# Kernel optimization log

Measured on AMD Instinct MI355X. Metric: run time of the kernel, lower is better.

Reference implementation:

```python
import jax, jax.numpy as jnp
import numpy as np

N, E = 30000, 480000
IN_DIM, HID, HEADS, OUT_DIM, EDIM = 128, 64, 4, 32, 1
NEG_SLOPE = 0.2
EPS_BN = 1e-5


def segment_softmax(logits, seg, num_segments):
    m = jax.ops.segment_max(logits, seg, num_segments=num_segments)
    ex = jnp.exp(logits - m[seg])
    s = jax.ops.segment_sum(ex, seg, num_segments=num_segments)
    return ex / (s[seg] + 1e-16)


def gat_layer(x, src, dst, ea, W, We, a_s, a_d, a_e, b):
    # PyG GATConv: shared lin for src/dst, edge_dim attention, softmax over dst
    n = x.shape[0]
    H, D = a_s.shape
    h = (x @ W).reshape(n, H, D)                      # [N,H,D]
    e = (ea @ We).reshape(-1, H, D)                   # [E,H,D]
    logits = (h * a_s).sum(-1)[src] + (h * a_d).sum(-1)[dst] + (e * a_e).sum(-1)
    alpha = segment_softmax(jax.nn.leaky_relu(logits, NEG_SLOPE), dst, n)  # [E,H]
    out = jax.ops.segment_sum(alpha[:, :, None] * h[src], dst, num_segments=n)
    return out.reshape(n, H * D) + b


def setup_inputs() -> dict:
    key = jax.random.key(0)
    ks = jax.random.split(key, 24)
    s = 0.1
    return {
        "x": jax.random.normal(ks[0], (N, IN_DIM), jnp.float32),
        "edge_attr": jax.random.uniform(ks[1], (E, EDIM), jnp.float32),
        "bn_gamma": jnp.ones((EDIM,), jnp.float32),
        "bn_beta": jnp.zeros((EDIM,), jnp.float32),
        "W1": s * jax.random.normal(ks[2], (IN_DIM, HEADS * HID), jnp.float32),
        "We1": s * jax.random.normal(ks[3], (EDIM, HEADS * HID), jnp.float32),
        "a_src1": s * jax.random.normal(ks[4], (HEADS, HID), jnp.float32),
        "a_dst1": s * jax.random.normal(ks[5], (HEADS, HID), jnp.float32),
        "a_edge1": s * jax.random.normal(ks[6], (HEADS, HID), jnp.float32),
        "b1": jnp.zeros((HEADS * HID,), jnp.float32),
        "W2": s * jax.random.normal(ks[7], (HEADS * HID, OUT_DIM), jnp.float32),
        "We2": s * jax.random.normal(ks[8], (EDIM, OUT_DIM), jnp.float32),
        "a_src2": s * jax.random.normal(ks[9], (1, OUT_DIM), jnp.float32),
        "a_dst2": s * jax.random.normal(ks[10], (1, OUT_DIM), jnp.float32),
        "a_edge2": s * jax.random.normal(ks[11], (1, OUT_DIM), jnp.float32),
        "b2": jnp.zeros((OUT_DIM,), jnp.float32),
        "dec_W1": s * jax.random.normal(ks[12], (OUT_DIM, HID), jnp.float32),
        "dec_b1": jnp.zeros((HID,), jnp.float32),
        "dec_W2": s * jax.random.normal(ks[13], (HID, IN_DIM), jnp.float32),
        "dec_b2": jnp.zeros((IN_DIM,), jnp.float32),
        "edge_index": jax.random.randint(ks[14], (2, E), 0, N, dtype=jnp.int32),
    }


def reference(x, edge_attr, bn_gamma, bn_beta, W1, We1, a_src1, a_dst1, a_edge1, b1,
              W2, We2, a_src2, a_dst2, a_edge2, b2, dec_W1, dec_b1, dec_W2, dec_b2,
              edge_index):
    n = x.shape[0]
    src, dst = edge_index[0], edge_index[1]
    # BatchNorm1d (batch stats, biased var) on log1p(edge_attr)
    ea = jnp.log1p(edge_attr)
    mu = ea.mean(0)
    var = ea.var(0)
    ea = (ea - mu) / jnp.sqrt(var + EPS_BN) * bn_gamma + bn_beta
    # add_self_loops with fill_value='mean' (mean of incoming edge attrs per node)
    ones = jnp.ones((src.shape[0],), ea.dtype)
    cnt = jax.ops.segment_sum(ones, dst, num_segments=n)
    loop_attr = jax.ops.segment_sum(ea, dst, num_segments=n) / jnp.maximum(cnt, 1.0)[:, None]
    ar = jnp.arange(n)
    src2 = jnp.concatenate([src, ar])
    dst2 = jnp.concatenate([dst, ar])
    ea2 = jnp.concatenate([ea, loop_attr], axis=0)
    # encoder: 2-layer GAT (eval mode: dropout is identity)
    h = jax.nn.elu(gat_layer(x, src2, dst2, ea2, W1, We1, a_src1, a_dst1, a_edge1, b1))
    z = gat_layer(h, src2, dst2, ea2, W2, We2, a_src2, a_dst2, a_edge2, b2)
    # feature decoder MLP
    x_hat = jax.nn.elu(z @ dec_W1 + dec_b1) @ dec_W2 + dec_b2
    return z, x_hat
```

## Files before the change

### kernel.cpp

```cpp
#include <hip/hip_runtime.h>
#include <math.h>

#define NN 30000
#define EE 480000
#define NEG_SLOPE 0.2f
#define LDK 136
#define LDK2 264
#define CAP 64

static const size_t I_FILL  = 0;
static const size_t F_PART  = 30000;
static const size_t F_SCAL  = 31024;
static const size_t F_WTB   = 31040;
static const size_t F_WT2B  = 47424;
static const size_t F_HB    = 51520;
static const size_t F_S1    = 3891520;
static const size_t F_D1    = 4011520;
static const size_t F_H1B   = 4131520;
static const size_t F_H2    = 7971520;
static const size_t F_S2    = 8931520;
static const size_t F_D2    = 8961520;
static const size_t I_ER    = 8991520;

typedef __attribute__((ext_vector_type(4))) float f32x4;
typedef __attribute__((ext_vector_type(8))) short bf16x8;

__device__ __forceinline__ float wsum64(float v) {
    #pragma unroll
    for (int o = 32; o; o >>= 1) v += __shfl_xor(v, o);
    return v;
}
__device__ __forceinline__ unsigned int pack_bf2(float a, float b) {
    unsigned int ua = __float_as_uint(a);
    unsigned int ub = __float_as_uint(b);
    ua = (ua + 0x7FFFu + ((ua >> 16) & 1u)) >> 16;
    ub = (ub + 0x7FFFu + ((ub >> 16) & 1u)) & 0xFFFF0000u;
    return ua | ub;
}
__device__ __forceinline__ unsigned short bf16r(float f) {
    unsigned int u = __float_as_uint(f);
    u = (u + 0x7FFFu + ((u >> 16) & 1u)) >> 16;
    return (unsigned short)u;
}
__device__ __forceinline__ float bflo(unsigned int u) { return __uint_as_float(u << 16); }
__device__ __forceinline__ float bfhi(unsigned int u) { return __uint_as_float(u & 0xFFFF0000u); }

__global__ __launch_bounds__(256) void k_prepw(const float* __restrict__ W1,
        const float* __restrict__ W2, unsigned short* __restrict__ wtb,
        unsigned short* __restrict__ wt2b, int* __restrict__ fill) {
    int idx = blockIdx.x * 256 + threadIdx.x;
    if (idx < NN) fill[idx] = 0;
    if (idx < 128 * 256) {
        int k = idx >> 8, n = idx & 255;
        wtb[n * 128 + k] = bf16r(W1[idx]);
    } else if (idx < 128 * 256 + 256 * 32) {
        int i2 = idx - 128 * 256;
        int k = i2 >> 5, c = i2 & 31;
        wt2b[c * 256 + k] = bf16r(W2[i2]);
    }
}

__global__ __launch_bounds__(256) void k_bn(const float* __restrict__ ea,
        float* __restrict__ part, int E) {
    __shared__ float sa[256], sb[256];
    int tid = threadIdx.x;
    float s = 0.f, s2 = 0.f;
    for (int i = blockIdx.x * 256 + tid; i < E; i += gridDim.x * 256) {
        float v = log1pf(ea[i]);
        s += v; s2 += v * v;
    }
    sa[tid] = s; sb[tid] = s2;
    __syncthreads();
    for (int o = 128; o; o >>= 1) {
        if (tid < o) { sa[tid] += sa[tid + o]; sb[tid] += sb[tid + o]; }
        __syncthreads();
    }
    if (tid == 0) { part[blockIdx.x * 2] = sa[0]; part[blockIdx.x * 2 + 1] = sb[0]; }
}

__global__ __launch_bounds__(512) void k_bn_final(const float* __restrict__ part,
        const float* __restrict__ gamma, const float* __restrict__ beta,
        const float* __restrict__ We1, const float* __restrict__ ae1,
        const float* __restrict__ We2, const float* __restrict__ ae2,
        float* __restrict__ scal, int E) {
    __shared__ float sa[512], sb[512], sc[256];
    int tid = threadIdx.x;
    sa[tid] = part[2 * tid]; sb[tid] = part[2 * tid + 1];
    if (tid < 256) sc[tid] = We1[tid] * ae1[tid];
    __syncthreads();
    for (int o = 256; o; o >>= 1) {
        if (tid < o) { sa[tid] += sa[tid + o]; sb[tid] += sb[tid + o]; }
        __syncthreads();
    }
    if (tid == 0) {
        float mu = sa[0] / (float)E;
        float var = sb[0] / (float)E - mu * mu;
        float kA = gamma[0] / sqrtf(var + 1e-5f);
        scal[0] = kA; scal[1] = beta[0] - mu * kA;
        for (int h = 0; h < 4; h++) {
            float s = 0.f;
            for (int d = 0; d < 64; d++) s += sc[h * 64 + d];
            scal[4 + h] = s;
        }
        float s2 = 0.f;
        for (int d = 0; d < 32; d++) s2 += We2[d] * ae2[d];
        scal[8] = s2;
    }
}

__global__ __launch_bounds__(256) void k_scatter(const int* __restrict__ src,
        const int* __restrict__ dst, const float* __restrict__ eattr,
        const float* __restrict__ scal, int* __restrict__ fill,
        uint2* __restrict__ er, int E) {
    int e = blockIdx.x * 256 + threadIdx.x;
    if (e >= E) return;
    float v = log1pf(eattr[e]) * scal[0] + scal[1];
    int d = dst[e];
    int pos = atomicAdd(&fill[d], 1);
    if (pos > CAP - 2) pos = CAP - 2;
    er[d * CAP + pos] = make_uint2((unsigned int)src[e], __float_as_uint(v));
}

__global__ __launch_bounds__(256) void k_gemm1(const float* __restrict__ x,
        const unsigned short* __restrict__ wtb, const float* __restrict__ as1,
        const float* __restrict__ ad1, unsigned short* __restrict__ hb,
        float* __restrict__ s1, float* __restrict__ d1, int M) {
    __shared__ unsigned short xs[32 * LDK];
    __shared__ unsigned short wt[256 * LDK];
    int tid = threadIdx.x;
    int bm = blockIdx.x * 32;
    #pragma unroll
    for (int i = 0; i < 16; i++) {
        int c = tid + i * 256;
        int row = c >> 4, koff = (c & 15) * 8;
        uint4 v = *(const uint4*)&wtb[row * 128 + koff];
        *(uint4*)&wt[row * LDK + koff] = v;
    }
    #pragma unroll
    for (int i = 0; i < 4; i++) {
        int idx = tid + i * 256;
        int row = idx >> 5, c4 = (idx & 31) * 4;
        int grow = bm + row;
        float4 v = make_float4(0.f, 0.f, 0.f, 0.f);
        if (grow < M) v = *(const float4*)&x[grow * 128 + c4];
        uint2 p = make_uint2(pack_bf2(v.x, v.y), pack_bf2(v.z, v.w));
        *(uint2*)&xs[row * LDK + c4] = p;
    }
    __syncthreads();

    int w = tid >> 6;
    int l = tid & 63;
    int l15 = l & 15, lg = l >> 4;

    f32x4 acc[2][4];
    #pragma unroll
    for (int m = 0; m < 2; m++)
        #pragma unroll
        for (int n = 0; n < 4; n++) acc[m][n] = (f32x4){0.f, 0.f, 0.f, 0.f};

    #pragma unroll
    for (int ks = 0; ks < 4; ks++) {
        int k0 = ks * 32 + lg * 8;
        bf16x8 a0 = *(const bf16x8*)&xs[(l15) * LDK + k0];
        bf16x8 a1 = *(const bf16x8*)&xs[(16 + l15) * LDK + k0];
        bf16x8 b[4];
        #pragma unroll
        for (int n = 0; n < 4; n++)
            b[n] = *(const bf16x8*)&wt[(w * 64 + n * 16 + l15) * LDK + k0];
        #pragma unroll
        for (int n = 0; n < 4; n++) {
            acc[0][n] = __builtin_amdgcn_mfma_f32_16x16x32_bf16(a0, b[n], acc[0][n], 0, 0, 0);
            acc[1][n] = __builtin_amdgcn_mfma_f32_16x16x32_bf16(a1, b[n], acc[1][n], 0, 0, 0);
        }
    }

    #pragma unroll
    for (int m = 0; m < 2; m++) {
        #pragma unroll
        for (int r = 0; r < 4; r++) {
            int grow = bm + m * 16 + lg * 4 + r;
            if (grow < M) {
                #pragma unroll
                for (int n = 0; n < 4; n++)
                    hb[grow * 256 + w * 64 + n * 16 + l15] = bf16r(acc[m][n][r]);
            }
        }
    }
    float as_c[4], ad_c[4];
    #pragma unroll
    for (int n = 0; n < 4; n++) {
        as_c[n] = as1[w * 64 + n * 16 + l15];
        ad_c[n] = ad1[w * 64 + n * 16 + l15];
    }
    float sp[2][4], dp[2][4];
    #pragma unroll
    for (int m = 0; m < 2; m++)
        #pragma unroll
        for (int r = 0; r < 4; r++) {
            float s = 0.f, d = 0.f;
            #pragma unroll
            for (int n = 0; n < 4; n++) {
                s += acc[m][n][r] * as_c[n];
                d += acc[m][n][r] * ad_c[n];
            }
            sp[m][r] = s; dp[m][r] = d;
        }
    #pragma unroll
    for (int o = 1; o < 16; o <<= 1) {
        #pragma unroll
        for (int m = 0; m < 2; m++)
            #pragma unroll
            for (int r = 0; r < 4; r++) {
                sp[m][r] += __shfl_xor(sp[m][r], o);
                dp[m][r] += __shfl_xor(dp[m][r], o);
            }
    }
    if (l15 == 0) {
        #pragma unroll
        for (int m = 0; m < 2; m++)
            #pragma unroll
            for (int r = 0; r < 4; r++) {
                int grow = bm + m * 16 + lg * 4 + r;
                if (grow < M) {
                    s1[grow * 4 + w] = sp[m][r];
                    d1[grow * 4 + w] = dp[m][r];
                }
            }
    }
}

__global__ __launch_bounds__(256) void k_agg1(const int* __restrict__ fill,
        const uint2* __restrict__ er, const float* __restrict__ s1,
        const float* __restrict__ d1, const float* __restrict__ scal,
        const unsigned short* __restrict__ hb, const float* __restrict__ b1,
        unsigned short* __restrict__ h1b, int N) {
    __shared__ float sma[4][256];
    __shared__ int   sms[4][64];
    int wid = threadIdx.x >> 6;
    int node = blockIdx.x * 4 + wid;
    if (node >= N) return;
    int lane = threadIdx.x & 63;
    int deg = fill[node]; if (deg > 63) deg = 63;
    float4 dv = *(const float4*)&d1[node * 4];
    float4 ce = *(const float4*)&scal[4];

    uint2 e = make_uint2((unsigned int)node, 0u);
    if (lane < deg) e = er[node * CAP + lane];
    float ev = (lane < deg) ? __uint_as_float(e.y) : 0.f;
    float evm = wsum64(ev) / fmaxf((float)deg, 1.f);
    int degT = deg + 1;
    if (lane == deg) ev = evm;
    bool valid = lane < degT;

    float4 l = make_float4(-1e30f, -1e30f, -1e30f, -1e30f);
    if (valid) {
        float4 sv = *(const float4*)&s1[e.x * 4];
        l.x = sv.x + dv.x + ev * ce.x;
        l.y = sv.y + dv.y + ev * ce.y;
        l.z = sv.z + dv.z + ev * ce.z;
        l.w = sv.w + dv.w + ev * ce.w;
        l.x = l.x > 0.f ? l.x : NEG_SLOPE * l.x;
        l.y = l.y > 0.f ? l.y : NEG_SLOPE * l.y;
        l.z = l.z > 0.f ? l.z : NEG_SLOPE * l.z;
        l.w = l.w > 0.f ? l.w : NEG_SLOPE * l.w;
    }
    float4 mx = l;
    #pragma unroll
    for (int o = 32; o; o >>= 1) {
        mx.x = fmaxf(mx.x, __shfl_xor(mx.x, o));
        mx.y = fmaxf(mx.y, __shfl_xor(mx.y, o));
        mx.z = fmaxf(mx.z, __shfl_xor(mx.z, o));
        mx.w = fmaxf(mx.w, __shfl_xor(mx.w, o));
    }
    float4 ex = make_float4(0.f, 0.f, 0.f, 0.f);
    if (valid) {
        ex.x = __expf(l.x - mx.x); ex.y = __expf(l.y - mx.y);
        ex.z = __expf(l.z - mx.z); ex.w = __expf(l.w - mx.w);
    }
    float4 sm = ex;
    #pragma unroll
    for (int o = 32; o; o >>= 1) {
        sm.x += __shfl_xor(sm.x, o); sm.y += __shfl_xor(sm.y, o);
        sm.z += __shfl_xor(sm.z, o); sm.w += __shfl_xor(sm.w, o);
    }
    *(float4*)&sma[wid][lane * 4] = make_float4(ex.x, ex.y, ex.z, ex.w);
    sms[wid][lane] = (int)e.x;
    int p = lane >> 5;
    int dL = lane & 31;
    int h = dL >> 3;
    float acc[8];
    #pragma unroll
    for (int i = 0; i < 8; i++) acc[i] = 0.f;
    for (int c0 = 0; c0 < degT; c0 += 8) {
        int sv[4]; float av[4];
        #pragma unroll
        for (int t = 0; t < 4; t++) {
            int ee = c0 + 2 * t + p;
            sv[t] = sms[wid][ee];
            av[t] = sma[wid][ee * 4 + h];
        }
        uint4 hv[4];
        #pragma unroll
        for (int t = 0; t < 4; t++)
            hv[t] = *(const uint4*)&hb[(unsigned)sv[t] * 256 + dL * 8];
        #pragma unroll
        for (int t = 0; t < 4; t++) {
            float a = av[t];
            acc[0] += a * bflo(hv[t].x); acc[1] += a * bfhi(hv[t].x);
            acc[2] += a * bflo(hv[t].y); acc[3] += a * bfhi(hv[t].y);
            acc[4] += a * bflo(hv[t].z); acc[5] += a * bfhi(hv[t].z);
            acc[6] += a * bflo(hv[t].w); acc[7] += a * bfhi(hv[t].w);
        }
    }
    #pragma unroll
    for (int i = 0; i < 8; i++) acc[i] += __shfl_xor(acc[i], 32);
    float smh = h == 0 ? sm.x : h == 1 ? sm.y : h == 2 ? sm.z : sm.w;
    float invh = 1.f / (smh + 1e-16f);
    float4 bb0 = *(const float4*)&b1[dL * 8];
    float4 bb1 = *(const float4*)&b1[dL * 8 + 4];
    float r[8];
    r[0] = acc[0] * invh + bb0.x; r[1] = acc[1] * invh + bb0.y;
    r[2] = acc[2] * invh + bb0.z; r[3] = acc[3] * invh + bb0.w;
    r[4] = acc[4] * invh + bb1.x; r[5] = acc[5] * invh + bb1.y;
    r[6] = acc[6] * invh + bb1.z; r[7] = acc[7] * invh + bb1.w;
    #pragma unroll
    for (int i = 0; i < 8; i++)
        r[i] = r[i] > 0.f ? r[i] : (__expf(r[i]) - 1.f);
    if (p == 0) {
        uint4 pk;
        pk.x = pack_bf2(r[0], r[1]); pk.y = pack_bf2(r[2], r[3]);
        pk.z = pack_bf2(r[4], r[5]); pk.w = pack_bf2(r[6], r[7]);
        *(uint4*)&h1b[node * 256 + dL * 8] = pk;
    }
}

__global__ __launch_bounds__(256) void k_gemm2(const unsigned short* __restrict__ h1b,
        const unsigned short* __restrict__ wt2b, const float* __restrict__ as2,
        const float* __restrict__ ad2, float* __restrict__ h2,
        float* __restrict__ s2, float* __restrict__ d2, int M) {
    __shared__ unsigned short h1s[64 * LDK2];
    __shared__ unsigned short w2s[32 * LDK2];
    int tid = threadIdx.x;
    int bm = blockIdx.x * 64;
    #pragma unroll
    for (int i = 0; i < 8; i++) {
        int c = tid + i * 256;
        int row = c >> 5, off = (c & 31) * 8;
        int grow = bm + row;
        uint4 v = make_uint4(0u, 0u, 0u, 0u);
        if (grow < M) v = *(const uint4*)&h1b[grow * 256 + off];
        *(uint4*)&h1s[row * LDK2 + off] = v;
    }
    #pragma unroll
    for (int i = 0; i < 4; i++) {
        int c = tid + i * 256;
        int row = c >> 5, off = (c & 31) * 8;
        uint4 v = *(const uint4*)&wt2b[row * 256 + off];
        *(uint4*)&w2s[row * LDK2 + off] = v;
    }
    __syncthreads();

    int w = tid >> 6;
    int l = tid & 63;
    int l15 = l & 15, lg = l >> 4;

    f32x4 acc0 = (f32x4){0.f, 0.f, 0.f, 0.f};
    f32x4 acc1 = (f32x4){0.f, 0.f, 0.f, 0.f};
    #pragma unroll
    for (int ks = 0; ks < 8; ks++) {
        int k0 = ks * 32 + lg * 8;
        bf16x8 a = *(const bf16x8*)&h1s[(w * 16 + l15) * LDK2 + k0];
        bf16x8 b0 = *(const bf16x8*)&w2s[(l15) * LDK2 + k0];
        bf16x8 b1 = *(const bf16x8*)&w2s[(16 + l15) * LDK2 + k0];
        acc0 = __builtin_amdgcn_mfma_f32_16x16x32_bf16(a, b0, acc0, 0, 0, 0);
        acc1 = __builtin_amdgcn_mfma_f32_16x16x32_bf16(a, b1, acc1, 0, 0, 0);
    }

    #pragma unroll
    for (int r = 0; r < 4; r++) {
        int grow = bm + w * 16 + lg * 4 + r;
        if (grow < M) {
            h2[grow * 32 + l15] = acc0[r];
            h2[grow * 32 + 16 + l15] = acc1[r];
        }
    }
    float sc0 = as2[l15], sc1 = as2[16 + l15];
    float dc0 = ad2[l15], dc1 = ad2[16 + l15];
    #pragma unroll
    for (int r = 0; r < 4; r++) {
        float sp = acc0[r] * sc0 + acc1[r] * sc1;
        float dp = acc0[r] * dc0 + acc1[r] * dc1;
        #pragma unroll
        for (int o = 1; o < 16; o <<= 1) {
            sp += __shfl_xor(sp, o);
            dp += __shfl_xor(dp, o);
        }
        if (l15 == 0) {
            int grow = bm + w * 16 + lg * 4 + r;
            if (grow < M) { s2[grow] = sp; d2[grow] = dp; }
        }
    }
}

__global__ __launch_bounds__(256) void k_agg2(const int* __restrict__ fill,
        const uint2* __restrict__ er, const float* __restrict__ s2,
        const float* __restrict__ d2, const float* __restrict__ scal,
        const float* __restrict__ h2, const float* __restrict__ b2,
        float* __restrict__ zout, int N) {
    __shared__ float sa2[4][64];
    __shared__ int   ss2[4][64];
    int wid = threadIdx.x >> 6;
    int node = blockIdx.x * 4 + wid;
    if (node >= N) return;
    int lane = threadIdx.x & 63;
    int deg = fill[node]; if (deg > 63) deg = 63;
    float dn = d2[node];
    float ce = scal[8];

    uint2 e = make_uint2((unsigned int)node, 0u);
    if (lane < deg) e = er[node * CAP + lane];
    float ev = (lane < deg) ? __uint_as_float(e.y) : 0.f;
    float evm = wsum64(ev) / fmaxf((float)deg, 1.f);
    int degT = deg + 1;
    if (lane == deg) ev = evm;
    bool valid = lane < degT;

    float l = -1e30f;
    if (valid) {
        l = s2[e.x] + dn + ev * ce;
        l = l > 0.f ? l : NEG_SLOPE * l;
    }
    float mx = l;
    #pragma unroll
    for (int o = 32; o; o >>= 1) mx = fmaxf(mx, __shfl_xor(mx, o));
    float ex = valid ? __expf(l - mx) : 0.f;
    float sm = wsum64(ex);
    float inv = 1.f / (sm + 1e-16f);
    sa2[wid][lane] = ex;
    ss2[wid][lane] = (int)e.x;
    int p8 = lane >> 3, dL2 = lane & 7;
    float4 acc = make_float4(0.f, 0.f, 0.f, 0.f);
    for (int c0 = 0; c0 < degT; c0 += 32) {
        int sv[4]; float av[4];
        #pragma unroll
        for (int t = 0; t < 4; t++) {
            int ee = c0 + 8 * t + p8;
            sv[t] = ss2[wid][ee];
            av[t] = sa2[wid][ee];
        }
        float4 hv[4];
        #pragma unroll
        for (int t = 0; t < 4; t++)
            hv[t] = *(const float4*)&h2[(unsigned)sv[t] * 32 + dL2 * 4];
        #pragma unroll
        for (int t = 0; t < 4; t++) {
            acc.x += av[t] * hv[t].x; acc.y += av[t] * hv[t].y;
            acc.z += av[t] * hv[t].z; acc.w += av[t] * hv[t].w;
        }
    }
    #pragma unroll
    for (int o = 8; o <= 32; o <<= 1) {
        acc.x += __shfl_xor(acc.x, o); acc.y += __shfl_xor(acc.y, o);
        acc.z += __shfl_xor(acc.z, o); acc.w += __shfl_xor(acc.w, o);
    }
    if (lane < 8) {
        float4 bb = *(const float4*)&b2[dL2 * 4];
        float4 oo;
        oo.x = acc.x * inv + bb.x; oo.y = acc.y * inv + bb.y;
        oo.z = acc.z * inv + bb.z; oo.w = acc.w * inv + bb.w;
        *(float4*)&zout[node * 32 + dL2 * 4] = oo;
    }
}

__global__ __launch_bounds__(256) void k_decoder(const float* __restrict__ z,
        const float* __restrict__ W1, const float* __restrict__ b1,
        const float* __restrict__ W2, const float* __restrict__ b2,
        float* __restrict__ xhat, int M) {
    __shared__ float zs[16][32];
    __shared__ float w1s[32 * 64];
    __shared__ float hid[16][68];
    __shared__ float w2s[64 * 128];
    int tid = threadIdx.x;
    int bn = blockIdx.x * 16;
    #pragma unroll
    for (int i = 0; i < 2; i++) {
        int idx = tid + i * 256;
        int r = idx >> 5, c = idx & 31;
        int row = bn + r;
        zs[r][c] = (row < M) ? z[row * 32 + c] : 0.f;
    }
    #pragma unroll
    for (int i = 0; i < 2; i++) {
        int idx = tid + i * 256;
        int r = idx >> 4, c = (idx & 15) * 4;
        *(float4*)&w1s[r * 64 + c] = *(const float4*)&W1[r * 64 + c];
    }
    #pragma unroll
    for (int i = 0; i < 8; i++) {
        int idx = tid + i * 256;
        int r = idx >> 5, c = (idx & 31) * 4;
        *(float4*)&w2s[r * 128 + c] = *(const float4*)&W2[r * 128 + c];
    }
    __syncthreads();
    {
        int nl = tid >> 4, c0 = (tid & 15) * 4;
        float4 acc = make_float4(0.f, 0.f, 0.f, 0.f);
        #pragma unroll 8
        for (int k = 0; k < 32; k++) {
            float zv = zs[nl][k];
            float4 w = *(float4*)&w1s[k * 64 + c0];
            acc.x += zv * w.x; acc.y += zv * w.y;
            acc.z += zv * w.z; acc.w += zv * w.w;
        }
        float4 bb = *(const float4*)&b1[c0];
        float r0 = acc.x + bb.x, r1 = acc.y + bb.y, r2 = acc.z + bb.z, r3 = acc.w + bb.w;
        r0 = r0 > 0.f ? r0 : (__expf(r0) - 1.f);
        r1 = r1 > 0.f ? r1 : (__expf(r1) - 1.f);
        r2 = r2 > 0.f ? r2 : (__expf(r2) - 1.f);
        r3 = r3 > 0.f ? r3 : (__expf(r3) - 1.f);
        hid[nl][c0] = r0; hid[nl][c0 + 1] = r1; hid[nl][c0 + 2] = r2; hid[nl][c0 + 3] = r3;
    }
    __syncthreads();
    {
        int nl = tid >> 4, c0 = (tid & 15) * 4;
        float acc[8];
        #pragma unroll
        for (int q = 0; q < 8; q++) acc[q] = 0.f;
        #pragma unroll 8
        for (int k = 0; k < 64; k++) {
            float hv = hid[nl][k];
            float4 w0 = *(float4*)&w2s[k * 128 + c0];
            float4 w1 = *(float4*)&w2s[k * 128 + c0 + 64];
            acc[0] += hv * w0.x; acc[1] += hv * w0.y; acc[2] += hv * w0.z; acc[3] += hv * w0.w;
            acc[4] += hv * w1.x; acc[5] += hv * w1.y; acc[6] += hv * w1.z; acc[7] += hv * w1.w;
        }
        int row = bn + nl;
        if (row < M) {
            float4 bb0 = *(const float4*)&b2[c0];
            float4 bb1 = *(const float4*)&b2[c0 + 64];
            float4 o0 = make_float4(acc[0] + bb0.x, acc[1] + bb0.y, acc[2] + bb0.z, acc[3] + bb0.w);
            float4 o1 = make_float4(acc[4] + bb1.x, acc[5] + bb1.y, acc[6] + bb1.z, acc[7] + bb1.w);
            *(float4*)&xhat[row * 128 + c0] = o0;
            *(float4*)&xhat[row * 128 + c0 + 64] = o1;
        }
    }
}

extern "C" void kernel_launch(void* const* d_in, const int* in_sizes, int n_in,
                              void* d_out, int out_size, void* d_ws, size_t ws_size,
                              hipStream_t stream) {
    const float* x        = (const float*)d_in[0];
    const float* eattr    = (const float*)d_in[1];
    const float* bn_gamma = (const float*)d_in[2];
    const float* bn_beta  = (const float*)d_in[3];
    const float* W1       = (const float*)d_in[4];
    const float* We1      = (const float*)d_in[5];
    const float* as1      = (const float*)d_in[6];
    const float* ad1      = (const float*)d_in[7];
    const float* ae1      = (const float*)d_in[8];
    const float* b1       = (const float*)d_in[9];
    const float* W2       = (const float*)d_in[10];
    const float* We2      = (const float*)d_in[11];
    const float* as2      = (const float*)d_in[12];
    const float* ad2      = (const float*)d_in[13];
    const float* ae2      = (const float*)d_in[14];
    const float* b2       = (const float*)d_in[15];
    const float* dW1      = (const float*)d_in[16];
    const float* db1      = (const float*)d_in[17];
    const float* dW2      = (const float*)d_in[18];
    const float* db2      = (const float*)d_in[19];
    const int*   eidx     = (const int*)d_in[20];
    const int* src = eidx;
    const int* dst = eidx + EE;

    float* ws = (float*)d_ws;
    int*   fill = (int*)(ws + I_FILL);
    float* part = ws + F_PART;
    float* scal = ws + F_SCAL;
    unsigned short* wtb  = (unsigned short*)(ws + F_WTB);
    unsigned short* wt2b = (unsigned short*)(ws + F_WT2B);
    unsigned short* hb   = (unsigned short*)(ws + F_HB);
    float* s1   = ws + F_S1;
    float* d1   = ws + F_D1;
    unsigned short* h1b = (unsigned short*)(ws + F_H1B);
    float* h2   = ws + F_H2;
    float* s2   = ws + F_S2;
    float* d2   = ws + F_D2;
    uint2* er   = (uint2*)(ws + I_ER);

    float* zout = (float*)d_out;
    float* xhat = (float*)d_out + NN * 32;

    k_prepw<<<160, 256, 0, stream>>>(W1, W2, wtb, wt2b, fill);
    k_bn<<<512, 256, 0, stream>>>(eattr, part, EE);
    k_bn_final<<<1, 512, 0, stream>>>(part, bn_gamma, bn_beta, We1, ae1, We2, ae2, scal, EE);
    k_scatter<<<(EE + 255) / 256, 256, 0, stream>>>(src, dst, eattr, scal, fill, er, EE);
    k_gemm1<<<(NN + 31) / 32, 256, 0, stream>>>(x, wtb, as1, ad1, hb, s1, d1, NN);
    k_agg1<<<(NN + 3) / 4, 256, 0, stream>>>(fill, er, s1, d1, scal, hb, b1, h1b, NN);
    k_gemm2<<<(NN + 63) / 64, 256, 0, stream>>>(h1b, wt2b, as2, ad2, h2, s2, d2, NN);
    k_agg2<<<(NN + 3) / 4, 256, 0, stream>>>(fill, er, s2, d2, scal, h2, b2, zout, NN);
    k_decoder<<<(NN + 15) / 16, 256, 0, stream>>>(zout, dW1, db1, dW2, db2, xhat, NN);
}
```

Baseline: 139.4 us.

## Fuse BN stats into scatter pass and prefetch neighbor rows in aggregation

```diff
diff --git a/kernel.cpp b/kernel.cpp
--- a/kernel.cpp
+++ b/kernel.cpp
@@ -7,20 +7,21 @@
 #define LDK 136
 #define LDK2 264
 #define CAP 64
+#define NPB 1875
 
 static const size_t I_FILL  = 0;
 static const size_t F_PART  = 30000;
-static const size_t F_SCAL  = 31024;
-static const size_t F_WTB   = 31040;
-static const size_t F_WT2B  = 47424;
-static const size_t F_HB    = 51520;
-static const size_t F_S1    = 3891520;
-static const size_t F_D1    = 4011520;
-static const size_t F_H1B   = 4131520;
-static const size_t F_H2    = 7971520;
-static const size_t F_S2    = 8931520;
-static const size_t F_D2    = 8961520;
-static const size_t I_ER    = 8991520;
+static const size_t F_SCAL  = 34096;
+static const size_t F_WTB   = 34112;
+static const size_t F_WT2B  = 50496;
+static const size_t F_HB    = 54592;
+static const size_t F_S1    = 3894592;
+static const size_t F_D1    = 4014592;
+static const size_t F_H1B   = 4134592;
+static const size_t F_H2    = 7974592;
+static const size_t F_S2    = 8934592;
+static const size_t F_D2    = 8964592;
+static const size_t I_ER    = 8994592;
 
 typedef __attribute__((ext_vector_type(4))) float f32x4;
 typedef __attribute__((ext_vector_type(8))) short bf16x8;
@@ -60,14 +61,21 @@
     }
 }
 
-__global__ __launch_bounds__(256) void k_bn(const float* __restrict__ ea,
+__global__ __launch_bounds__(256) void k_scatter(const int* __restrict__ src,
+        const int* __restrict__ dst, const float* __restrict__ eattr,
+        int* __restrict__ fill, uint2* __restrict__ er,
         float* __restrict__ part, int E) {
     __shared__ float sa[256], sb[256];
     int tid = threadIdx.x;
+    int e = blockIdx.x * 256 + tid;
     float s = 0.f, s2 = 0.f;
-    for (int i = blockIdx.x * 256 + tid; i < E; i += gridDim.x * 256) {
-        float v = log1pf(ea[i]);
-        s += v; s2 += v * v;
+    if (e < E) {
+        float lv = log1pf(eattr[e]);
+        s = lv; s2 = lv * lv;
+        int d = dst[e];
+        int pos = atomicAdd(&fill[d], 1);
+        if (pos > CAP - 2) pos = CAP - 2;
+        er[d * CAP + pos] = make_uint2((unsigned int)src[e], __float_as_uint(lv));
     }
     sa[tid] = s; sb[tid] = s2;
     __syncthreads();
@@ -85,7 +93,11 @@
         float* __restrict__ scal, int E) {
     __shared__ float sa[512], sb[512], sc[256];
     int tid = threadIdx.x;
-    sa[tid] = part[2 * tid]; sb[tid] = part[2 * tid + 1];
+    float s = 0.f, s2 = 0.f;
+    for (int i = tid; i < NPB; i += 512) {
+        s += part[2 * i]; s2 += part[2 * i + 1];
+    }
+    sa[tid] = s; sb[tid] = s2;
     if (tid < 256) sc[tid] = We1[tid] * ae1[tid];
     __syncthreads();
     for (int o = 256; o; o >>= 1) {
@@ -96,29 +108,18 @@
         float mu = sa[0] / (float)E;
         float var = sb[0] / (float)E - mu * mu;
         float kA = gamma[0] / sqrtf(var + 1e-5f);
-        scal[0] = kA; scal[1] = beta[0] - mu * kA;
+        float kB = beta[0] - mu * kA;
         for (int h = 0; h < 4; h++) {
-            float s = 0.f;
-            for (int d = 0; d < 64; d++) s += sc[h * 64 + d];
-            scal[4 + h] = s;
-        }
-        float s2 = 0.f;
-        for (int d = 0; d < 32; d++) s2 += We2[d] * ae2[d];
-        scal[8] = s2;
-    }
-}
-
-__global__ __launch_bounds__(256) void k_scatter(const int* __restrict__ src,
-        const int* __restrict__ dst, const float* __restrict__ eattr,
-        const float* __restrict__ scal, int* __restrict__ fill,
-        uint2* __restrict__ er, int E) {
-    int e = blockIdx.x * 256 + threadIdx.x;
-    if (e >= E) return;
-    float v = log1pf(eattr[e]) * scal[0] + scal[1];
-    int d = dst[e];
-    int pos = atomicAdd(&fill[d], 1);
-    if (pos > CAP - 2) pos = CAP - 2;
-    er[d * CAP + pos] = make_uint2((unsigned int)src[e], __float_as_uint(v));
+            float s1 = 0.f;
+            for (int d = 0; d < 64; d++) s1 += sc[h * 64 + d];
+            scal[4 + h] = kA * s1;
+            scal[10 + h] = kB * s1;
+        }
+        float s22 = 0.f;
+        for (int d = 0; d < 32; d++) s22 += We2[d] * ae2[d];
+        scal[8] = kA * s22;
+        scal[9] = kB * s22;
+    }
 }
 
 __global__ __launch_bounds__(256) void k_gemm1(const float* __restrict__ x,
@@ -243,6 +244,7 @@
     int deg = fill[node]; if (deg > 63) deg = 63;
     float4 dv = *(const float4*)&d1[node * 4];
     float4 ce = *(const float4*)&scal[4];
+    float4 cc = *(const float4*)&scal[10];
 
     uint2 e = make_uint2((unsigned int)node, 0u);
     if (lane < deg) e = er[node * CAP + lane];
@@ -252,13 +254,25 @@
     if (lane == deg) ev = evm;
     bool valid = lane < degT;
 
+    sms[wid][lane] = (int)e.x;
+    int p = lane >> 5;
+    int dL = lane & 31;
+    int h = dL >> 3;
+    uint4 hv[12];
+    #pragma unroll
+    for (int t = 0; t < 12; t++) {
+        int ee = 2 * t + p;
+        if (ee < degT)
+            hv[t] = *(const uint4*)&hb[(unsigned)sms[wid][ee] * 256 + dL * 8];
+    }
+
     float4 l = make_float4(-1e30f, -1e30f, -1e30f, -1e30f);
     if (valid) {
         float4 sv = *(const float4*)&s1[e.x * 4];
-        l.x = sv.x + dv.x + ev * ce.x;
-        l.y = sv.y + dv.y + ev * ce.y;
-        l.z = sv.z + dv.z + ev * ce.z;
-        l.w = sv.w + dv.w + ev * ce.w;
+        l.x = sv.x + dv.x + ev * ce.x + cc.x;
+        l.y = sv.y + dv.y + ev * ce.y + cc.y;
+        l.z = sv.z + dv.z + ev * ce.z + cc.z;
+        l.w = sv.w + dv.w + ev * ce.w + cc.w;
         l.x = l.x > 0.f ? l.x : NEG_SLOPE * l.x;
         l.y = l.y > 0.f ? l.y : NEG_SLOPE * l.y;
         l.z = l.z > 0.f ? l.z : NEG_SLOPE * l.z;
@@ -284,32 +298,34 @@
         sm.z += __shfl_xor(sm.z, o); sm.w += __shfl_xor(sm.w, o);
     }
     *(float4*)&sma[wid][lane * 4] = make_float4(ex.x, ex.y, ex.z, ex.w);
-    sms[wid][lane] = (int)e.x;
-    int p = lane >> 5;
-    int dL = lane & 31;
-    int h = dL >> 3;
+
     float acc[8];
     #pragma unroll
     for (int i = 0; i < 8; i++) acc[i] = 0.f;
-    for (int c0 = 0; c0 < degT; c0 += 8) {
-        int sv[4]; float av[4];
-        #pragma unroll
-        for (int t = 0; t < 4; t++) {
-            int ee = c0 + 2 * t + p;
-            sv[t] = sms[wid][ee];
-            av[t] = sma[wid][ee * 4 + h];
-        }
-        uint4 hv[4];
-        #pragma unroll
-        for (int t = 0; t < 4; t++)
-            hv[t] = *(const uint4*)&hb[(unsigned)sv[t] * 256 + dL * 8];
-        #pragma unroll
-        for (int t = 0; t < 4; t++) {
-            float a = av[t];
+    #pragma unroll
+    for (int t = 0; t < 12; t++) {
+        int ee = 2 * t + p;
+        if (ee < degT) {
+            float a = sma[wid][ee * 4 + h];
             acc[0] += a * bflo(hv[t].x); acc[1] += a * bfhi(hv[t].x);
             acc[2] += a * bflo(hv[t].y); acc[3] += a * bfhi(hv[t].y);
             acc[4] += a * bflo(hv[t].z); acc[5] += a * bfhi(hv[t].z);
             acc[6] += a * bflo(hv[t].w); acc[7] += a * bfhi(hv[t].w);
+        }
+    }
+    for (int c0 = 24; c0 < degT; c0 += 8) {
+        #pragma unroll
+        for (int t = 0; t < 4; t++) {
+            int ee = c0 + 2 * t + p;
+            if (ee < degT) {
+                int sv = sms[wid][ee];
+                float a = sma[wid][ee * 4 + h];
+                uint4 hh = *(const uint4*)&hb[(unsigned)sv * 256 + dL * 8];
+                acc[0] += a * bflo(hh.x); acc[1] += a * bfhi(hh.x);
+                acc[2] += a * bflo(hh.y); acc[3] += a * bfhi(hh.y);
+                acc[4] += a * bflo(hh.z); acc[5] += a * bfhi(hh.z);
+                acc[6] += a * bflo(hh.w); acc[7] += a * bfhi(hh.w);
+            }
         }
     }
     #pragma unroll
@@ -415,7 +431,7 @@
     int lane = threadIdx.x & 63;
     int deg = fill[node]; if (deg > 63) deg = 63;
     float dn = d2[node];
-    float ce = scal[8];
+    float ce = scal[8], cc = scal[9];
 
     uint2 e = make_uint2((unsigned int)node, 0u);
     if (lane < deg) e = er[node * CAP + lane];
@@ -425,9 +441,19 @@
     if (lane == deg) ev = evm;
     bool valid = lane < degT;
 
+    ss2[wid][lane] = (int)e.x;
+    int p8 = lane >> 3, dL2 = lane & 7;
+    float4 hv[3];
+    #pragma unroll
+    for (int t = 0; t < 3; t++) {
+        int ee = 8 * t + p8;
+        if (ee < degT)
+            hv[t] = *(const float4*)&h2[(unsigned)ss2[wid][ee] * 32 + dL2 * 4];
+    }
+
     float l = -1e30f;
     if (valid) {
-        l = s2[e.x] + dn + ev * ce;
+        l = s2[e.x] + dn + ev * ce + cc;
         l = l > 0.f ? l : NEG_SLOPE * l;
     }
     float mx = l;
@@ -437,25 +463,24 @@
     float sm = wsum64(ex);
     float inv = 1.f / (sm + 1e-16f);
     sa2[wid][lane] = ex;
-    ss2[wid][lane] = (int)e.x;
-    int p8 = lane >> 3, dL2 = lane & 7;
+
     float4 acc = make_float4(0.f, 0.f, 0.f, 0.f);
-    for (int c0 = 0; c0 < degT; c0 += 32) {
-        int sv[4]; float av[4];
-        #pragma unroll
-        for (int t = 0; t < 4; t++) {
-            int ee = c0 + 8 * t + p8;
-            sv[t] = ss2[wid][ee];
-            av[t] = sa2[wid][ee];
-        }
-        float4 hv[4];
-        #pragma unroll
-        for (int t = 0; t < 4; t++)
-            hv[t] = *(const float4*)&h2[(unsigned)sv[t] * 32 + dL2 * 4];
-        #pragma unroll
-        for (int t = 0; t < 4; t++) {
-            acc.x += av[t] * hv[t].x; acc.y += av[t] * hv[t].y;
-            acc.z += av[t] * hv[t].z; acc.w += av[t] * hv[t].w;
+    #pragma unroll
+    for (int t = 0; t < 3; t++) {
+        int ee = 8 * t + p8;
+        if (ee < degT) {
+            float a = sa2[wid][ee];
+            acc.x += a * hv[t].x; acc.y += a * hv[t].y;
+            acc.z += a * hv[t].z; acc.w += a * hv[t].w;
+        }
+    }
+    for (int c0 = 24; c0 < degT; c0 += 8) {
+        int ee = c0 + p8;
+        if (ee < degT) {
+            float a = sa2[wid][ee];
+            float4 hh = *(const float4*)&h2[(unsigned)ss2[wid][ee] * 32 + dL2 * 4];
+            acc.x += a * hh.x; acc.y += a * hh.y;
+            acc.z += a * hh.z; acc.w += a * hh.w;
         }
     }
     #pragma unroll
@@ -592,9 +617,8 @@
     float* xhat = (float*)d_out + NN * 32;
 
     k_prepw<<<160, 256, 0, stream>>>(W1, W2, wtb, wt2b, fill);
-    k_bn<<<512, 256, 0, stream>>>(eattr, part, EE);
+    k_scatter<<<NPB, 256, 0, stream>>>(src, dst, eattr, fill, er, part, EE);
     k_bn_final<<<1, 512, 0, stream>>>(part, bn_gamma, bn_beta, We1, ae1, We2, ae2, scal, EE);
-    k_scatter<<<(EE + 255) / 256, 256, 0, stream>>>(src, dst, eattr, scal, fill, er, EE);
     k_gemm1<<<(NN + 31) / 32, 256, 0, stream>>>(x, wtb, as1, ad1, hb, s1, d1, NN);
     k_agg1<<<(NN + 3) / 4, 256, 0, stream>>>(fill, er, s1, d1, scal, hb, b1, h1b, NN);
     k_gemm2<<<(NN + 63) / 64, 256, 0, stream>>>(h1b, wt2b, as2, ad2, h2, s2, d2, NN);
```

Measured after the change: 141.0 us. Within noise of the previous version (+1.2%).
